# Kernel optimization log

Measured on AMD Instinct MI355X. Metric: run time of the kernel, lower is better.

The kernel has to match this reference:

```python
import jax, jax.numpy as jnp
from jax import lax
import numpy as np

B, S, HID = 1, 1024, 4096
H, D = 64, 64  # num_heads, head_size (hidden = H*D)


def setup_inputs() -> dict:
    key = jax.random.key(0)
    ks = jax.random.split(key, 14)
    s = 0.02  # weight init scale
    return {
        "hidden": jax.random.normal(ks[0], (B, S, HID), jnp.float32),
        "w_key": jax.random.normal(ks[1], (HID, HID), jnp.float32) * s,
        "w_value": jax.random.normal(ks[2], (HID, HID), jnp.float32) * s,
        "w_receptance": jax.random.normal(ks[3], (HID, HID), jnp.float32) * s,
        "w_gate": jax.random.normal(ks[4], (HID, HID), jnp.float32) * s,
        "w_output": jax.random.normal(ks[5], (HID, HID), jnp.float32) * s,
        "time_mix_key": jax.random.uniform(ks[6], (HID,), jnp.float32),
        "time_mix_value": jax.random.uniform(ks[7], (HID,), jnp.float32),
        "time_mix_receptance": jax.random.uniform(ks[8], (HID,), jnp.float32),
        "time_mix_gate": jax.random.uniform(ks[9], (HID,), jnp.float32),
        "time_decay": jax.random.normal(ks[10], (H, D), jnp.float32) * 0.5,
        "time_faaaa": jax.random.normal(ks[11], (H, D), jnp.float32) * 0.5,
        "gn_weight": jnp.ones((HID,), jnp.float32),
        "gn_bias": jnp.zeros((HID,), jnp.float32),
    }


def reference(hidden, w_key, w_value, w_receptance, w_gate, w_output,
              time_mix_key, time_mix_value, time_mix_receptance, time_mix_gate,
              time_decay, time_faaaa, gn_weight, gn_bias):
    b, s, hid = hidden.shape
    h, d = time_decay.shape

    # time_shift: shifted[t] = hidden[t-1], shifted[0] = 0 (state is None)
    shifted = jnp.concatenate([jnp.zeros_like(hidden[:, :1]), hidden[:, :-1]], axis=1)

    def mix(m):
        return hidden * m + shifted * (1.0 - m)

    k = mix(time_mix_key) @ w_key.T            # (b, s, hid)
    v = mix(time_mix_value) @ w_value.T
    r = mix(time_mix_receptance) @ w_receptance.T
    g = jax.nn.silu(mix(time_mix_gate) @ w_gate.T)

    def heads(x):  # (b, s, hid) -> (s, b, h, d) for scan over time
        return x.reshape(b, s, h, d).transpose(1, 0, 2, 3)

    kh, vh, rh = heads(k), heads(v), heads(r)

    td = jnp.exp(-jnp.exp(time_decay))[None, :, :, None]  # (1, h, d, 1)
    tf = time_faaaa[None, :, :, None]                      # (1, h, d, 1)

    def step(state, rkv):
        r_t, k_t, v_t = rkv                                # each (b, h, d)
        a = k_t[..., :, None] * v_t[..., None, :]          # (b, h, d, d) outer product
        o = jnp.einsum('bhd,bhde->bhe', r_t, tf * a + state)
        return a + td * state, o

    state0 = jnp.zeros((b, h, d, d), jnp.float32)
    _, out = lax.scan(step, state0, (rh, kh, vh))          # out: (s, b, h, d)
    out = out.transpose(1, 0, 2, 3).reshape(b, s, hid)

    # GroupNorm(num_groups=h, channels=hid) over flattened tokens
    x = out.reshape(b * s, h, d)
    mu = x.mean(-1, keepdims=True)
    var = x.var(-1, keepdims=True)
    xn = (x - mu) * lax.rsqrt(var + 1e-5)
    xn = xn.reshape(b * s, hid) * gn_weight + gn_bias
    xn = xn.reshape(b, s, hid)

    return (g * xn) @ w_output.T
```

## Files before the change

### kernel.cpp

```cpp
#include <hip/hip_runtime.h>

#define S_LEN 1024
#define HIDN  4096
#define NH    64
#define HD    64
#define NCH   32
#define CLEN  32

typedef short bf16x8 __attribute__((ext_vector_type(8)));
typedef float f32x4  __attribute__((ext_vector_type(4)));

__device__ __forceinline__ unsigned short f2bf(float x){
  unsigned u = __float_as_uint(x);
  u += 0x7fffu + ((u >> 16) & 1u);
  return (unsigned short)(u >> 16);
}

__device__ __forceinline__ void gload_lds16(const void* g, void* l){
  __builtin_amdgcn_global_load_lds(
      (const __attribute__((address_space(1))) void*)g,
      (__attribute__((address_space(3))) void*)l, 16, 0, 0);
}

__global__ __launch_bounds__(256)
void wconv_kernel(const float* __restrict__ w0, const float* __restrict__ w1,
                  const float* __restrict__ w2, const float* __restrict__ w3,
                  const float* __restrict__ w4, unsigned short* __restrict__ out)
{
  const int z = blockIdx.y;
  const float* __restrict__ w = (z==0)?w0:(z==1)?w1:(z==2)?w2:(z==3)?w3:w4;
  const size_t idx = (size_t)blockIdx.x * 2048 + (size_t)threadIdx.x * 8;
  float4 a = *(const float4*)(w + idx);
  float4 b = *(const float4*)(w + idx + 4);
  ushort4 lo, hi;
  lo.x = f2bf(a.x); lo.y = f2bf(a.y); lo.z = f2bf(a.z); lo.w = f2bf(a.w);
  hi.x = f2bf(b.x); hi.y = f2bf(b.y); hi.z = f2bf(b.z); hi.w = f2bf(b.w);
  unsigned short* o = out + (size_t)z * HIDN * HIDN + idx;
  *(ushort4*)(o)     = lo;
  *(ushort4*)(o + 4) = hi;
}

__global__ __launch_bounds__(256)
void mix_kernel(const float* __restrict__ hidden,
                const float* __restrict__ tmk, const float* __restrict__ tmv,
                const float* __restrict__ tmr, const float* __restrict__ tmg,
                unsigned short* __restrict__ mixed)
{
  int idx = blockIdx.x * 256 + threadIdx.x;
  int i = idx & (HIDN - 1);
  float h  = hidden[idx];
  float sh = (idx >= HIDN) ? hidden[idx - HIDN] : 0.f;
  float mk = tmk[i], mv = tmv[i], mr = tmr[i], mg = tmg[i];
  mixed[idx + 0 * S_LEN * HIDN] = f2bf(h * mk + sh * (1.f - mk));
  mixed[idx + 1 * S_LEN * HIDN] = f2bf(h * mv + sh * (1.f - mv));
  mixed[idx + 2 * S_LEN * HIDN] = f2bf(h * mr + sh * (1.f - mr));
  mixed[idx + 3 * S_LEN * HIDN] = f2bf(h * mg + sh * (1.f - mg));
}

__global__ __launch_bounds__(256)
void gemm_lds(const unsigned short* __restrict__ Aall,
              const unsigned short* __restrict__ Wall,
              float* __restrict__ Call, int silu_mask, int nzper)
{
  const int bid  = blockIdx.x;
  const int xcd  = bid & 7;
  const int slot = bid >> 3;
  const int mt   = slot & 7;
  const int nz   = xcd * nzper + (slot >> 3);
  const int nt   = nz & 31;
  const int z    = nz >> 5;

  const unsigned short* __restrict__ A = Aall + (size_t)z * S_LEN * HIDN;
  const unsigned short* __restrict__ W = Wall + (size_t)z * HIDN * HIDN;
  float* __restrict__ C = Call + (size_t)z * S_LEN * HIDN;
  const int m0 = mt * 128;
  const int n0 = nt * 128;

  __shared__ unsigned short As[2][128 * 32];
  __shared__ unsigned short Bs[2][128 * 32];

  const int tid  = threadIdx.x;
  const int lane = tid & 63;
  const int wave = tid >> 6;
  const int wr = (wave >> 1) * 64;
  const int wc = (wave & 1) * 64;
  const int fr = lane & 15;
  const int fk = (lane >> 4) * 8;

  const int q0 = tid, q1 = 256 + tid;
  const int r0 = q0 >> 2, c0 = (q0 & 3) * 8;
  const int r1 = q1 >> 2, c1 = (q1 & 3) * 8;
  const unsigned short* A0 = A + (size_t)(m0 + r0) * HIDN + c0;
  const unsigned short* A1 = A + (size_t)(m0 + r1) * HIDN + c1;
  const unsigned short* W0 = W + (size_t)(n0 + r0) * HIDN + c0;
  const unsigned short* W1 = W + (size_t)(n0 + r1) * HIDN + c1;

  f32x4 acc[4][4];
#pragma unroll
  for (int mi = 0; mi < 4; ++mi)
#pragma unroll
    for (int ni = 0; ni < 4; ++ni) acc[mi][ni] = (f32x4){0.f, 0.f, 0.f, 0.f};

  for (int k0 = 0; k0 < HIDN; k0 += 64) {
    gload_lds16(A0 + k0,      &As[0][q0 * 8]);
    gload_lds16(A1 + k0,      &As[0][q1 * 8]);
    gload_lds16(A0 + k0 + 32, &As[1][q0 * 8]);
    gload_lds16(A1 + k0 + 32, &As[1][q1 * 8]);
    gload_lds16(W0 + k0,      &Bs[0][q0 * 8]);
    gload_lds16(W1 + k0,      &Bs[0][q1 * 8]);
    gload_lds16(W0 + k0 + 32, &Bs[1][q0 * 8]);
    gload_lds16(W1 + k0 + 32, &Bs[1][q1 * 8]);
    __syncthreads();

#pragma unroll
    for (int kk = 0; kk < 2; ++kk) {
      bf16x8 af[4], bq[4];
#pragma unroll
      for (int mi = 0; mi < 4; ++mi)
        af[mi] = *(const bf16x8*)(&As[kk][(wr + mi * 16 + fr) * 32 + fk]);
#pragma unroll
      for (int ni = 0; ni < 4; ++ni)
        bq[ni] = *(const bf16x8*)(&Bs[kk][(wc + ni * 16 + fr) * 32 + fk]);
#pragma unroll
      for (int mi = 0; mi < 4; ++mi)
#pragma unroll
        for (int ni = 0; ni < 4; ++ni)
          acc[mi][ni] = __builtin_amdgcn_mfma_f32_16x16x32_bf16(af[mi], bq[ni], acc[mi][ni], 0, 0, 0);
    }
    __syncthreads();
  }

  const bool do_silu = (silu_mask >> z) & 1;
  const int orow = (lane >> 4) * 4;
#pragma unroll
  for (int mi = 0; mi < 4; ++mi)
#pragma unroll
    for (int ni = 0; ni < 4; ++ni)
#pragma unroll
      for (int r = 0; r < 4; ++r) {
        int row = m0 + wr + mi * 16 + orow + r;
        int col = n0 + wc + ni * 16 + fr;
        float v = acc[mi][ni][r];
        if (do_silu) v = v / (1.f + __expf(-v));
        C[(size_t)row * HIDN + col] = v;
      }
}

__global__ __launch_bounds__(256)
void gemm_splitk(const unsigned short* __restrict__ A,
                 const unsigned short* __restrict__ W,
                 float* __restrict__ C)
{
  const int bid  = blockIdx.x;
  const int xcd  = bid & 7;
  const int slot = bid >> 3;
  const int mt   = slot & 7;
  const int nl   = (slot >> 3) & 3;
  const int ks   = slot >> 5;
  const int nt   = xcd * 4 + nl;
  const int m0 = mt * 128, n0 = nt * 128;
  const int kb = ks * (HIDN / 2), ke = kb + (HIDN / 2);

  __shared__ unsigned short As[2][128 * 32];
  __shared__ unsigned short Bs[2][128 * 32];

  const int tid  = threadIdx.x;
  const int lane = tid & 63;
  const int wave = tid >> 6;
  const int wr = (wave >> 1) * 64;
  const int wc = (wave & 1) * 64;
  const int fr = lane & 15;
  const int fk = (lane >> 4) * 8;

  const int q0 = tid, q1 = 256 + tid;
  const int r0 = q0 >> 2, c0 = (q0 & 3) * 8;
  const int r1 = q1 >> 2, c1 = (q1 & 3) * 8;
  const unsigned short* A0 = A + (size_t)(m0 + r0) * HIDN + c0;
  const unsigned short* A1 = A + (size_t)(m0 + r1) * HIDN + c1;
  const unsigned short* W0 = W + (size_t)(n0 + r0) * HIDN + c0;
  const unsigned short* W1 = W + (size_t)(n0 + r1) * HIDN + c1;

  f32x4 acc[4][4];
#pragma unroll
  for (int mi = 0; mi < 4; ++mi)
#pragma unroll
    for (int ni = 0; ni < 4; ++ni) acc[mi][ni] = (f32x4){0.f, 0.f, 0.f, 0.f};

  for (int k0 = kb; k0 < ke; k0 += 64) {
    gload_lds16(A0 + k0,      &As[0][q0 * 8]);
    gload_lds16(A1 + k0,      &As[0][q1 * 8]);
    gload_lds16(A0 + k0 + 32, &As[1][q0 * 8]);
    gload_lds16(A1 + k0 + 32, &As[1][q1 * 8]);
    gload_lds16(W0 + k0,      &Bs[0][q0 * 8]);
    gload_lds16(W1 + k0,      &Bs[0][q1 * 8]);
    gload_lds16(W0 + k0 + 32, &Bs[1][q0 * 8]);
    gload_lds16(W1 + k0 + 32, &Bs[1][q1 * 8]);
    __syncthreads();

#pragma unroll
    for (int kk = 0; kk < 2; ++kk) {
      bf16x8 af[4], bq[4];
#pragma unroll
      for (int mi = 0; mi < 4; ++mi)
        af[mi] = *(const bf16x8*)(&As[kk][(wr + mi * 16 + fr) * 32 + fk]);
#pragma unroll
      for (int ni = 0; ni < 4; ++ni)
        bq[ni] = *(const bf16x8*)(&Bs[kk][(wc + ni * 16 + fr) * 32 + fk]);
#pragma unroll
      for (int mi = 0; mi < 4; ++mi)
#pragma unroll
        for (int ni = 0; ni < 4; ++ni)
          acc[mi][ni] = __builtin_amdgcn_mfma_f32_16x16x32_bf16(af[mi], bq[ni], acc[mi][ni], 0, 0, 0);
    }
    __syncthreads();
  }

  const int orow = (lane >> 4) * 4;
#pragma unroll
  for (int mi = 0; mi < 4; ++mi)
#pragma unroll
    for (int ni = 0; ni < 4; ++ni)
#pragma unroll
      for (int r = 0; r < 4; ++r) {
        int row = m0 + wr + mi * 16 + orow + r;
        int col = n0 + wc + ni * 16 + fr;
        atomicAdd(&C[(size_t)row * HIDN + col], acc[mi][ni][r]);
      }
}

__global__ __launch_bounds__(64)
void rec_pass1(const float* __restrict__ kb, const float* __restrict__ vb,
               const float* __restrict__ time_decay, float* __restrict__ X)
{
  const int c = blockIdx.x, h = blockIdx.y, e = threadIdx.x;
  const float tde = __expf(-__expf(time_decay[h * 64 + e]));
  float td[64];
#pragma unroll
  for (int d = 0; d < 64; ++d) td[d] = __shfl(tde, d, 64);
  float st[64];
#pragma unroll
  for (int d = 0; d < 64; ++d) st[d] = 0.f;

  for (int t = c * CLEN; t < c * CLEN + CLEN; ++t) {
    const size_t off = (size_t)t * HIDN + h * 64;
    const float vl = vb[off + e];
    const float* __restrict__ krow = kb + off;
#pragma unroll
    for (int d = 0; d < 64; ++d)
      st[d] = fmaf(td[d], st[d], krow[d] * vl);
  }
#pragma unroll
  for (int d = 0; d < 64; ++d)
    X[(((size_t)c * NH + h) * 64 + d) * 64 + e] = st[d];
}

__global__ __launch_bounds__(64)
void rec_pass2(const float* __restrict__ time_decay,
               const float* __restrict__ X, float* __restrict__ Y)
{
  const int h = blockIdx.x, dq = blockIdx.y, e = threadIdx.x;
  float tdc[16];
#pragma unroll
  for (int i = 0; i < 16; ++i)
    tdc[i] = __expf(-(float)CLEN * __expf(time_decay[h * 64 + dq * 16 + i]));
  float acc[16];
#pragma unroll
  for (int i = 0; i < 16; ++i) acc[i] = 0.f;
  for (int c = 0; c < NCH; ++c) {
#pragma unroll
    for (int i = 0; i < 16; ++i) {
      size_t idx = (((size_t)c * NH + h) * 64 + dq * 16 + i) * 64 + e;
      Y[idx] = acc[i];
      acc[i] = fmaf(tdc[i], acc[i], X[idx]);
    }
  }
}

__global__ __launch_bounds__(64)
void rec_pass3(const float* __restrict__ kb, const float* __restrict__ vb,
               const float* __restrict__ rb, const float* __restrict__ gb,
               const float* __restrict__ time_decay, const float* __restrict__ time_faaaa,
               const float* __restrict__ gnw, const float* __restrict__ gnb,
               const float* __restrict__ Y, unsigned short* __restrict__ A2)
{
  const int c = blockIdx.x, h = blockIdx.y, e = threadIdx.x;
  const float tde = __expf(-__expf(time_decay[h * 64 + e]));
  float td[64];
#pragma unroll
  for (int d = 0; d < 64; ++d) td[d] = __shfl(tde, d, 64);
  float st[64];
#pragma unroll
  for (int d = 0; d < 64; ++d)
    st[d] = Y[(((size_t)c * NH + h) * 64 + d) * 64 + e];

  const float tf_l  = time_faaaa[h * 64 + e];
  const float gnw_l = gnw[h * 64 + e];
  const float gnb_l = gnb[h * 64 + e];

  for (int t = c * CLEN; t < c * CLEN + CLEN; ++t) {
    const size_t off = (size_t)t * HIDN + h * 64;
    const float kl = kb[off + e], rl = rb[off + e];
    const float vl = vb[off + e], gl = gb[off + e];

    float Asum = rl * tf_l * kl;
#pragma unroll
    for (int i = 1; i < 64; i <<= 1) Asum += __shfl_xor(Asum, i, 64);

    const float* __restrict__ krow = kb + off;
    const float* __restrict__ rrow = rb + off;
    float dot = 0.f;
#pragma unroll
    for (int d = 0; d < 64; ++d) {
      dot   = fmaf(rrow[d], st[d], dot);
      st[d] = fmaf(td[d], st[d], krow[d] * vl);
    }
    float o = fmaf(Asum, vl, dot);

    float s1 = o, s2 = o * o;
#pragma unroll
    for (int i = 1; i < 64; i <<= 1) {
      s1 += __shfl_xor(s1, i, 64);
      s2 += __shfl_xor(s2, i, 64);
    }
    float mean = s1 * (1.f / 64.f);
    float var  = s2 * (1.f / 64.f) - mean * mean;
    float xn   = (o - mean) * rsqrtf(var + 1e-5f);
    float yv   = xn * gnw_l + gnb_l;
    A2[off + e] = f2bf(gl * yv);
  }
}

extern "C" void kernel_launch(void* const* d_in, const int* in_sizes, int n_in,
                              void* d_out, int out_size, void* d_ws, size_t ws_size,
                              hipStream_t stream)
{
  const float* hidden     = (const float*)d_in[0];
  const float* w_key      = (const float*)d_in[1];
  const float* w_value    = (const float*)d_in[2];
  const float* w_recep    = (const float*)d_in[3];
  const float* w_gate     = (const float*)d_in[4];
  const float* w_output   = (const float*)d_in[5];
  const float* tmk        = (const float*)d_in[6];
  const float* tmv        = (const float*)d_in[7];
  const float* tmr        = (const float*)d_in[8];
  const float* tmg        = (const float*)d_in[9];
  const float* time_decay = (const float*)d_in[10];
  const float* time_faaaa = (const float*)d_in[11];
  const float* gnw        = (const float*)d_in[12];
  const float* gnb        = (const float*)d_in[13];
  float* out = (float*)d_out;

  char* ws = (char*)d_ws;
  unsigned short* wbf   = (unsigned short*)(ws);
  float*          Y     = (float*)(ws);
  unsigned short* mixed = (unsigned short*)(ws + 167772160);
  float*          X     = (float*)(ws + 167772160);
  float*          kvrg  = (float*)(ws + 201326592);
  unsigned short* A2    = (unsigned short*)(ws + 268435456);

  const float* kb = kvrg + 0 * (size_t)S_LEN * HIDN;
  const float* vb = kvrg + 1 * (size_t)S_LEN * HIDN;
  const float* rb = kvrg + 2 * (size_t)S_LEN * HIDN;
  const float* gb = kvrg + 3 * (size_t)S_LEN * HIDN;

  wconv_kernel<<<dim3(HIDN * HIDN / 2048, 5), 256, 0, stream>>>(
      w_key, w_value, w_recep, w_gate, w_output, wbf);

  mix_kernel<<<dim3(S_LEN * HIDN / 256), 256, 0, stream>>>(hidden, tmk, tmv, tmr, tmg, mixed);

  gemm_lds<<<dim3(1024), 256, 0, stream>>>(mixed, wbf, kvrg, 0x8, 16);

  rec_pass1<<<dim3(NCH, NH), 64, 0, stream>>>(kb, vb, time_decay, X);
  rec_pass2<<<dim3(NH, 4), 64, 0, stream>>>(time_decay, X, Y);
  rec_pass3<<<dim3(NCH, NH), 64, 0, stream>>>(kb, vb, rb, gb, time_decay, time_faaaa,
                                              gnw, gnb, Y, A2);

  hipMemsetAsync(d_out, 0, (size_t)out_size * sizeof(float), stream);
  gemm_splitk<<<dim3(512), 256, 0, stream>>>(A2, wbf + 4 * (size_t)HIDN * HIDN, out);
}
```

Measured before the change: 707.9 us.

## Replace projection GEMM with 256x256 tiled, swizzled, software-pipelined MFMA kernel

Rewrites the four fused K/V/R/G projection GEMMs to use 256x256 output tiles with 8 waves per block, XOR-swizzled LDS layout to avoid bank conflicts, and double-buffered global-to-LDS loads interleaved with MFMA quadrants using explicit waitcnt, sched barriers and priority bumps. The aim is higher data reuse per tile and overlap of memory traffic with matrix math, removing the two full syncs per K-step of the old kernel. It uses much more LDS and registers per block and launches only 256 blocks, which reduces parallelism and makes the kernel depend on hand-tuned ordering.

```diff
diff --git a/kernel.cpp b/kernel.cpp
--- a/kernel.cpp
+++ b/kernel.cpp
@@ -6,6 +6,7 @@
 #define HD    64
 #define NCH   32
 #define CLEN  32
+#define NKT   64
 
 typedef short bf16x8 __attribute__((ext_vector_type(8)));
 typedef float f32x4  __attribute__((ext_vector_type(4)));
@@ -21,6 +22,16 @@
       (const __attribute__((address_space(1))) void*)g,
       (__attribute__((address_space(3))) void*)l, 16, 0, 0);
 }
+
+#define SBAR() do { __builtin_amdgcn_sched_barrier(0); \
+                    __builtin_amdgcn_s_barrier();      \
+                    __builtin_amdgcn_sched_barrier(0); } while(0)
+#define WAIT_LGKM0() do { asm volatile("s_waitcnt lgkmcnt(0)" ::: "memory"); \
+                          __builtin_amdgcn_sched_barrier(0); } while(0)
+#define WAIT_VM4()  do { asm volatile("s_waitcnt vmcnt(4)" ::: "memory"); \
+                         __builtin_amdgcn_sched_barrier(0); } while(0)
+#define WAIT_VM0()  do { asm volatile("s_waitcnt vmcnt(0)" ::: "memory"); \
+                         __builtin_amdgcn_sched_barrier(0); } while(0)
 
 __global__ __launch_bounds__(256)
 void wconv_kernel(const float* __restrict__ w0, const float* __restrict__ w1,
@@ -57,89 +68,149 @@
   mixed[idx + 3 * S_LEN * HIDN] = f2bf(h * mg + sh * (1.f - mg));
 }
 
-__global__ __launch_bounds__(256)
-void gemm_lds(const unsigned short* __restrict__ Aall,
-              const unsigned short* __restrict__ Wall,
-              float* __restrict__ Call, int silu_mask, int nzper)
+__global__ __launch_bounds__(512, 2)
+void gemm256(const unsigned short* __restrict__ Aall,
+             const unsigned short* __restrict__ Wall,
+             float* __restrict__ Call, int silu_mask)
 {
   const int bid  = blockIdx.x;
   const int xcd  = bid & 7;
   const int slot = bid >> 3;
-  const int mt   = slot & 7;
-  const int nz   = xcd * nzper + (slot >> 3);
-  const int nt   = nz & 31;
-  const int z    = nz >> 5;
+  const int nz   = xcd * 8 + (slot >> 2);
+  const int mt   = slot & 3;
+  const int z    = nz >> 4;
+  const int nt   = nz & 15;
+  const int m0 = mt * 256, n0 = nt * 256;
 
   const unsigned short* __restrict__ A = Aall + (size_t)z * S_LEN * HIDN;
   const unsigned short* __restrict__ W = Wall + (size_t)z * HIDN * HIDN;
   float* __restrict__ C = Call + (size_t)z * S_LEN * HIDN;
-  const int m0 = mt * 128;
-  const int n0 = nt * 128;
-
-  __shared__ unsigned short As[2][128 * 32];
-  __shared__ unsigned short Bs[2][128 * 32];
+
+  __shared__ __align__(16) unsigned short As[2][2][128 * 64];
+  __shared__ __align__(16) unsigned short Bs[2][2][128 * 64];
 
   const int tid  = threadIdx.x;
   const int lane = tid & 63;
-  const int wave = tid >> 6;
-  const int wr = (wave >> 1) * 64;
-  const int wc = (wave & 1) * 64;
-  const int fr = lane & 15;
-  const int fk = (lane >> 4) * 8;
-
-  const int q0 = tid, q1 = 256 + tid;
-  const int r0 = q0 >> 2, c0 = (q0 & 3) * 8;
-  const int r1 = q1 >> 2, c1 = (q1 & 3) * 8;
-  const unsigned short* A0 = A + (size_t)(m0 + r0) * HIDN + c0;
-  const unsigned short* A1 = A + (size_t)(m0 + r1) * HIDN + c1;
-  const unsigned short* W0 = W + (size_t)(n0 + r0) * HIDN + c0;
-  const unsigned short* W1 = W + (size_t)(n0 + r1) * HIDN + c1;
-
-  f32x4 acc[4][4];
-#pragma unroll
-  for (int mi = 0; mi < 4; ++mi)
+  const int wid  = tid >> 6;
+  const int wr   = wid >> 2;
+  const int wc   = wid & 3;
+  const int fr   = lane & 15;
+  const int fku  = lane >> 4;
+  const int cxA  = fku * 16;
+
+  const int ob0 = tid * 16, ob1 = (512 + tid) * 16;
+  const int r0 = ob0 >> 7, r1 = ob1 >> 7;
+  const int cb0 = (ob0 & 127) ^ ((r0 & 7) << 4);
+  const int cb1 = (ob1 & 127) ^ ((r1 & 7) << 4);
+  const unsigned short* A0 = A + (size_t)(m0 + r0) * HIDN + (cb0 >> 1);
+  const unsigned short* A1 = A + (size_t)(m0 + r1) * HIDN + (cb1 >> 1);
+  const unsigned short* W0 = W + (size_t)(n0 + r0) * HIDN + (cb0 >> 1);
+  const unsigned short* W1 = W + (size_t)(n0 + r1) * HIDN + (cb1 >> 1);
+  const int lo0 = ob0 >> 1, lo1 = ob1 >> 1;
+
+  f32x4 acc[8][4];
+#pragma unroll
+  for (int mi = 0; mi < 8; ++mi)
 #pragma unroll
     for (int ni = 0; ni < 4; ++ni) acc[mi][ni] = (f32x4){0.f, 0.f, 0.f, 0.f};
 
-  for (int k0 = 0; k0 < HIDN; k0 += 64) {
-    gload_lds16(A0 + k0,      &As[0][q0 * 8]);
-    gload_lds16(A1 + k0,      &As[0][q1 * 8]);
-    gload_lds16(A0 + k0 + 32, &As[1][q0 * 8]);
-    gload_lds16(A1 + k0 + 32, &As[1][q1 * 8]);
-    gload_lds16(W0 + k0,      &Bs[0][q0 * 8]);
-    gload_lds16(W1 + k0,      &Bs[0][q1 * 8]);
-    gload_lds16(W0 + k0 + 32, &Bs[1][q0 * 8]);
-    gload_lds16(W1 + k0 + 32, &Bs[1][q1 * 8]);
-    __syncthreads();
-
-#pragma unroll
-    for (int kk = 0; kk < 2; ++kk) {
-      bf16x8 af[4], bq[4];
+  auto stageA = [&](int t, int h, int db) {
+    gload_lds16(A0 + (size_t)h * 128 * HIDN + t * 64, &As[db][h][lo0]);
+    gload_lds16(A1 + (size_t)h * 128 * HIDN + t * 64, &As[db][h][lo1]);
+  };
+  auto stageB = [&](int t, int h, int db) {
+    gload_lds16(W0 + (size_t)h * 128 * HIDN + t * 64, &Bs[db][h][lo0]);
+    gload_lds16(W1 + (size_t)h * 128 * HIDN + t * 64, &Bs[db][h][lo1]);
+  };
+  auto readA = [&](bf16x8 (&a)[2][4], int db, int mh) {
+#pragma unroll
+    for (int kk = 0; kk < 2; ++kk)
+#pragma unroll
+      for (int mi = 0; mi < 4; ++mi) {
+        int rr  = mh * 64 + mi * 16 + fr;
+        int byo = rr * 128 + ((kk * 64 + cxA) ^ ((rr & 7) << 4));
+        a[kk][mi] = *(const bf16x8*)((const char*)As[db][wr] + byo);
+      }
+  };
+  auto readB = [&](bf16x8 (&b)[2][2], int db, int nh) {
+#pragma unroll
+    for (int kk = 0; kk < 2; ++kk)
+#pragma unroll
+      for (int ni = 0; ni < 2; ++ni) {
+        int rr  = (wc & 1) * 64 + nh * 32 + ni * 16 + fr;
+        int byo = rr * 128 + ((kk * 64 + cxA) ^ ((rr & 7) << 4));
+        b[kk][ni] = *(const bf16x8*)((const char*)Bs[db][wc >> 1] + byo);
+      }
+  };
+  auto quad = [&](bf16x8 (&a)[2][4], bf16x8 (&b)[2][2], int mh, int nh) {
+#pragma unroll
+    for (int kk = 0; kk < 2; ++kk)
 #pragma unroll
       for (int mi = 0; mi < 4; ++mi)
-        af[mi] = *(const bf16x8*)(&As[kk][(wr + mi * 16 + fr) * 32 + fk]);
-#pragma unroll
-      for (int ni = 0; ni < 4; ++ni)
-        bq[ni] = *(const bf16x8*)(&Bs[kk][(wc + ni * 16 + fr) * 32 + fk]);
-#pragma unroll
-      for (int mi = 0; mi < 4; ++mi)
-#pragma unroll
-        for (int ni = 0; ni < 4; ++ni)
-          acc[mi][ni] = __builtin_amdgcn_mfma_f32_16x16x32_bf16(af[mi], bq[ni], acc[mi][ni], 0, 0, 0);
-    }
-    __syncthreads();
+#pragma unroll
+        for (int ni = 0; ni < 2; ++ni)
+          acc[mh * 4 + mi][nh * 2 + ni] = __builtin_amdgcn_mfma_f32_16x16x32_bf16(
+              a[kk][mi], b[kk][ni], acc[mh * 4 + mi][nh * 2 + ni], 0, 0, 0);
+  };
+
+  stageB(0, 0, 0); stageB(0, 1, 0);
+  stageA(0, 0, 0); stageA(0, 1, 0);
+  stageB(1, 0, 1); stageB(1, 1, 1);
+  WAIT_VM4();
+  SBAR();
+
+  bf16x8 a8[2][4], b0[2][2], b1[2][2];
+
+  for (int T = 0; T < NKT; ++T) {
+    const int db  = T & 1;
+    const int dbA = (T + 1) & 1;
+    const int tA  = (T + 1 < NKT) ? T + 1 : NKT - 1;
+    const int tB  = (T + 2 < NKT) ? T + 2 : NKT - 1;
+    readA(a8, db, 0);
+    readB(b0, db, 0);
+    stageA(tA, 0, dbA);
+    SBAR();
+    WAIT_LGKM0();
+    __builtin_amdgcn_s_setprio(1);
+    quad(a8, b0, 0, 0);
+    __builtin_amdgcn_s_setprio(0);
+    SBAR();
+    readB(b1, db, 1);
+    stageA(tA, 1, dbA);
+    SBAR();
+    WAIT_LGKM0();
+    __builtin_amdgcn_s_setprio(1);
+    quad(a8, b1, 0, 1);
+    __builtin_amdgcn_s_setprio(0);
+    SBAR();
+    readA(a8, db, 1);
+    stageB(tB, 0, db);
+    SBAR();
+    WAIT_LGKM0();
+    __builtin_amdgcn_s_setprio(1);
+    quad(a8, b1, 1, 1);
+    __builtin_amdgcn_s_setprio(0);
+    SBAR();
+    stageB(tB, 1, db);
+    WAIT_VM4();
+    SBAR();
+    __builtin_amdgcn_s_setprio(1);
+    quad(a8, b0, 1, 0);
+    __builtin_amdgcn_s_setprio(0);
+    SBAR();
   }
+  WAIT_VM0();
 
   const bool do_silu = (silu_mask >> z) & 1;
-  const int orow = (lane >> 4) * 4;
-#pragma unroll
-  for (int mi = 0; mi < 4; ++mi)
+  const int orow = fku * 4;
+#pragma unroll
+  for (int mi = 0; mi < 8; ++mi)
 #pragma unroll
     for (int ni = 0; ni < 4; ++ni)
 #pragma unroll
       for (int r = 0; r < 4; ++r) {
-        int row = m0 + wr + mi * 16 + orow + r;
-        int col = n0 + wc + ni * 16 + fr;
+        int row = m0 + wr * 128 + mi * 16 + orow + r;
+        int col = n0 + wc * 64 + ni * 16 + fr;
         float v = acc[mi][ni][r];
         if (do_silu) v = v / (1.f + __expf(-v));
         C[(size_t)row * HIDN + col] = v;
@@ -368,7 +439,7 @@
 
   mix_kernel<<<dim3(S_LEN * HIDN / 256), 256, 0, stream>>>(hidden, tmk, tmv, tmr, tmg, mixed);
 
-  gemm_lds<<<dim3(1024), 256, 0, stream>>>(mixed, wbf, kvrg, 0x8, 16);
+  gemm256<<<dim3(256), 512, 0, stream>>>(mixed, wbf, kvrg, 0x8);
 
   rec_pass1<<<dim3(NCH, NH), 64, 0, stream>>>(kb, vb, time_decay, X);
   rec_pass2<<<dim3(NH, 4), 64, 0, stream>>>(time_decay, X, Y);
```

After: 675.9 us. 1.05x faster.
